# Kernel optimization log

Measured on AMD Instinct MI355X. Metric: run time of the kernel, lower is better.

The kernel has to match this reference:

```python
import jax, jax.numpy as jnp
import numpy as np

EPS_MIN = 1e-8
EPS_MAX = 1.0


def setup_inputs() -> dict:
    key = jax.random.key(0)
    k0, k1, k2, k3 = jax.random.split(key, 4)
    B, H, NT, NV = 8, 16, 512, 576
    return {
        "attn_t_0": jax.random.uniform(k0, (B, H, NT, NV), dtype=jnp.float32),
        "attn_v_0": jax.random.uniform(k1, (B, H, NV, NT), dtype=jnp.float32),
        "attn_t_1": jax.random.uniform(k2, (B, H, NT, NV), dtype=jnp.float32),
        "attn_v_1": jax.random.uniform(k3, (B, H, NV, NT), dtype=jnp.float32),
    }


def _layer_loss(attn_t, attn_v):
    # Head-mean attention maps
    P_t = attn_t.mean(axis=1)  # (B, NT, NV)
    P_v = attn_v.mean(axis=1)  # (B, NV, NT)
    # Only the diagonals of P_t @ P_v and P_v @ P_t are used:
    # diag(A @ B)[b, i] = sum_k A[b, i, k] * B[b, k, i]
    text_diag = jnp.einsum('bik,bki->bi', P_t, P_v)    # (B, NT)
    vision_diag = jnp.einsum('bjk,bkj->bj', P_v, P_t)  # (B, NV)
    text_diag = jnp.clip(text_diag, EPS_MIN, EPS_MAX)
    vision_diag = jnp.clip(vision_diag, EPS_MIN, EPS_MAX)
    loss_text = -jnp.log(text_diag).mean()
    loss_vision = -jnp.log(vision_diag).mean()
    return (loss_text + loss_vision) * 0.5


def reference(attn_t_0, attn_v_0, attn_t_1, attn_v_1) -> jnp.ndarray:
    layers = [(attn_t_0, attn_v_0), (attn_t_1, attn_v_1)]
    total = jnp.float32(0.0)
    for at, av in layers:
        total = total + _layer_loss(at, av)
    return total / len(layers)
```

## Files before the change

### kernel.cpp

```cpp
#include <hip/hip_runtime.h>
#include <math.h>

constexpr int B  = 8;
constexpr int H  = 16;
constexpr int NT = 512;
constexpr int NV = 576;
constexpr int TILE = 64;
constexpr float INV_H2 = 1.0f / (float)(H * H);

constexpr int TEXT_N = 2 * B * NT;
constexpr int VIS_N  = 2 * B * NV;

__global__ void zero_ws_kernel(float* __restrict__ ws, int n) {
    int i = blockIdx.x * blockDim.x + threadIdx.x;
    if (i < n) ws[i] = 0.0f;
}

__global__ __launch_bounds__(256) void fused_diag_kernel(
    const float* __restrict__ t0, const float* __restrict__ v0,
    const float* __restrict__ t1, const float* __restrict__ v1,
    float* __restrict__ text_acc,
    float* __restrict__ vis_acc)
{
    const int ktile = blockIdx.x;
    const int itile = blockIdx.y;
    const int bz    = blockIdx.z;
    const int b     = bz & (B - 1);
    const int layer = bz >> 3;

    const float* __restrict__ T = layer ? t1 : t0;
    const float* __restrict__ V = layer ? v1 : v0;

    const int tid = threadIdx.x;
    const int c = tid & 15;
    const int g = tid >> 4;

    const int i0 = itile * TILE;
    const int k0 = ktile * TILE;

    const size_t tbase = (size_t)b * H * NT * NV + (size_t)i0 * NV + k0;
    const size_t vbase = (size_t)b * H * NV * NT + (size_t)k0 * NT + i0;

    float4 tacc[4];
    float4 vacc[4];
#pragma unroll
    for (int r = 0; r < 4; ++r) {
        tacc[r] = make_float4(0.f, 0.f, 0.f, 0.f);
        vacc[r] = make_float4(0.f, 0.f, 0.f, 0.f);
    }

    for (int h = 0; h < H; ++h) {
        const float* tp = T + tbase + (size_t)h * NT * NV;
        const float* vp = V + vbase + (size_t)h * NV * NT;
#pragma unroll
        for (int r = 0; r < 4; ++r) {
            const int row = g + 16 * r;
            const float4 tv = *(const float4*)(tp + (size_t)row * NV + 4 * c);
            const float4 vv = *(const float4*)(vp + (size_t)row * NT + 4 * c);
            tacc[r].x += tv.x; tacc[r].y += tv.y; tacc[r].z += tv.z; tacc[r].w += tv.w;
            vacc[r].x += vv.x; vacc[r].y += vv.y; vacc[r].z += vv.z; vacc[r].w += vv.w;
        }
    }

    __shared__ float vlds[TILE * 65];
    __shared__ float rowsum[TILE];
    __shared__ float colsum[TILE];

    if (tid < TILE) {
        rowsum[tid] = 0.0f;
        colsum[tid] = 0.0f;
    }

#pragma unroll
    for (int r = 0; r < 4; ++r) {
        const int kk = g + 16 * r;
        float* p = &vlds[kk * 65 + 4 * c];
        p[0] = vacc[r].x; p[1] = vacc[r].y; p[2] = vacc[r].z; p[3] = vacc[r].w;
    }
    __syncthreads();

    float colpart[4] = {0.f, 0.f, 0.f, 0.f};
#pragma unroll
    for (int r = 0; r < 4; ++r) {
        const int ii = g + 16 * r;
        const float tq[4] = {tacc[r].x, tacc[r].y, tacc[r].z, tacc[r].w};
        float rp = 0.f;
#pragma unroll
        for (int j = 0; j < 4; ++j) {
            const int kk = 4 * c + j;
            const float q = tq[j] * vlds[kk * 65 + ii];
            rp += q;
            colpart[j] += q;
        }
        atomicAdd(&rowsum[ii], rp);
    }
#pragma unroll
    for (int j = 0; j < 4; ++j) {
        atomicAdd(&colsum[4 * c + j], colpart[j]);
    }
    __syncthreads();

    const int lb = layer * B + b;
    if (tid < TILE) {
        atomicAdd(&text_acc[(size_t)lb * NT + i0 + tid], rowsum[tid] * INV_H2);
    } else if (tid < 2 * TILE) {
        const int kk = tid - TILE;
        atomicAdd(&vis_acc[(size_t)lb * NV + k0 + kk], colsum[kk] * INV_H2);
    }
}

__global__ __launch_bounds__(256) void finalize_kernel(
    const float* __restrict__ text_acc,
    const float* __restrict__ vis_acc,
    float* __restrict__ out)
{
    const int tid = threadIdx.x;
    const float wt = 0.25f / (float)(B * NT);
    const float wv = 0.25f / (float)(B * NV);

    float s = 0.f;
    for (int i = tid; i < TEXT_N; i += 256) {
        float x = text_acc[i];
        x = fminf(fmaxf(x, 1e-8f), 1.0f);
        s += -logf(x) * wt;
    }
    for (int i = tid; i < VIS_N; i += 256) {
        float x = vis_acc[i];
        x = fminf(fmaxf(x, 1e-8f), 1.0f);
        s += -logf(x) * wv;
    }

#pragma unroll
    for (int off = 32; off > 0; off >>= 1) s += __shfl_down(s, off, 64);

    __shared__ float wsum[4];
    if ((tid & 63) == 0) wsum[tid >> 6] = s;
    __syncthreads();
    if (tid == 0) out[0] = wsum[0] + wsum[1] + wsum[2] + wsum[3];
}

extern "C" void kernel_launch(void* const* d_in, const int* in_sizes, int n_in,
                              void* d_out, int out_size, void* d_ws, size_t ws_size,
                              hipStream_t stream) {
    const float* t0 = (const float*)d_in[0];
    const float* v0 = (const float*)d_in[1];
    const float* t1 = (const float*)d_in[2];
    const float* v1 = (const float*)d_in[3];

    float* text_acc = (float*)d_ws;
    float* vis_acc  = text_acc + TEXT_N;
    float* out      = (float*)d_out;

    {
        const int n = TEXT_N + VIS_N;
        zero_ws_kernel<<<(n + 255) / 256, 256, 0, stream>>>(text_acc, n);
    }

    {
        dim3 grid(NV / TILE, NT / TILE, 2 * B);
        fused_diag_kernel<<<grid, 256, 0, stream>>>(t0, v0, t1, v1, text_acc, vis_acc);
    }

    finalize_kernel<<<1, 256, 0, stream>>>(text_acc, vis_acc, out);
}
```

Baseline: 504.6 us.

## Split head-mean into separate streaming kernel before diagonal product

Head averaging is moved out of the tiled diagonal kernel into a dedicated kernel that streams each input contiguously and writes per-batch head sums to workspace. The diagonal kernel then loads just one precomputed tile per operand instead of looping over heads with strided tile loads. This trades an extra intermediate write/read and an extra launch for more coalesced, bandwidth-friendly reads of the large inputs.

```diff
diff --git a/kernel.cpp b/kernel.cpp
--- a/kernel.cpp
+++ b/kernel.cpp
@@ -6,8 +6,12 @@
 constexpr int NT = 512;
 constexpr int NV = 576;
 constexpr int TILE = 64;
+constexpr int M  = NT * NV;
+constexpr int M4 = M / 4;
+constexpr int OUT4_PER_TENSOR = B * M4;
 constexpr float INV_H2 = 1.0f / (float)(H * H);
 
+constexpr size_t P_FLOATS = (size_t)4 * B * M;
 constexpr int TEXT_N = 2 * B * NT;
 constexpr int VIS_N  = 2 * B * NV;
 
@@ -16,9 +20,34 @@
     if (i < n) ws[i] = 0.0f;
 }
 
-__global__ __launch_bounds__(256) void fused_diag_kernel(
-    const float* __restrict__ t0, const float* __restrict__ v0,
-    const float* __restrict__ t1, const float* __restrict__ v1,
+__global__ __launch_bounds__(256) void mean_kernel(
+    const float4* __restrict__ x0, const float4* __restrict__ x1,
+    const float4* __restrict__ x2, const float4* __restrict__ x3,
+    float4* __restrict__ p)
+{
+    const int o = blockIdx.x * blockDim.x + threadIdx.x;
+    const int t = blockIdx.y;
+    const float4* __restrict__ x = (t == 0) ? x0 : (t == 1) ? x1 : (t == 2) ? x2 : x3;
+
+    const int b  = o / M4;
+    const int m4 = o - b * M4;
+    const float4* __restrict__ src = x + (size_t)b * H * M4 + m4;
+
+    float4 s0 = make_float4(0.f, 0.f, 0.f, 0.f);
+    float4 s1 = make_float4(0.f, 0.f, 0.f, 0.f);
+#pragma unroll
+    for (int h = 0; h < H; h += 2) {
+        const float4 a = src[(size_t)h * M4];
+        const float4 c = src[(size_t)(h + 1) * M4];
+        s0.x += a.x; s0.y += a.y; s0.z += a.z; s0.w += a.w;
+        s1.x += c.x; s1.y += c.y; s1.z += c.z; s1.w += c.w;
+    }
+    s0.x += s1.x; s0.y += s1.y; s0.z += s1.z; s0.w += s1.w;
+    p[(size_t)t * OUT4_PER_TENSOR + o] = s0;
+}
+
+__global__ __launch_bounds__(256) void diag_kernel(
+    const float* __restrict__ P,
     float* __restrict__ text_acc,
     float* __restrict__ vis_acc)
 {
@@ -28,8 +57,8 @@
     const int b     = bz & (B - 1);
     const int layer = bz >> 3;
 
-    const float* __restrict__ T = layer ? t1 : t0;
-    const float* __restrict__ V = layer ? v1 : v0;
+    const float* __restrict__ Pt = P + (size_t)(2 * layer) * B * M + (size_t)b * M;
+    const float* __restrict__ Pv = P + (size_t)(2 * layer + 1) * B * M + (size_t)b * M;
 
     const int tid = threadIdx.x;
     const int c = tid & 15;
@@ -38,28 +67,13 @@
     const int i0 = itile * TILE;
     const int k0 = ktile * TILE;
 
-    const size_t tbase = (size_t)b * H * NT * NV + (size_t)i0 * NV + k0;
-    const size_t vbase = (size_t)b * H * NV * NT + (size_t)k0 * NT + i0;
-
     float4 tacc[4];
     float4 vacc[4];
 #pragma unroll
     for (int r = 0; r < 4; ++r) {
-        tacc[r] = make_float4(0.f, 0.f, 0.f, 0.f);
-        vacc[r] = make_float4(0.f, 0.f, 0.f, 0.f);
-    }
-
-    for (int h = 0; h < H; ++h) {
-        const float* tp = T + tbase + (size_t)h * NT * NV;
-        const float* vp = V + vbase + (size_t)h * NV * NT;
-#pragma unroll
-        for (int r = 0; r < 4; ++r) {
-            const int row = g + 16 * r;
-            const float4 tv = *(const float4*)(tp + (size_t)row * NV + 4 * c);
-            const float4 vv = *(const float4*)(vp + (size_t)row * NT + 4 * c);
-            tacc[r].x += tv.x; tacc[r].y += tv.y; tacc[r].z += tv.z; tacc[r].w += tv.w;
-            vacc[r].x += vv.x; vacc[r].y += vv.y; vacc[r].z += vv.z; vacc[r].w += vv.w;
-        }
+        const int row = g + 16 * r;
+        tacc[r] = *(const float4*)(Pt + (size_t)(i0 + row) * NV + k0 + 4 * c);
+        vacc[r] = *(const float4*)(Pv + (size_t)(k0 + row) * NT + i0 + 4 * c);
     }
 
     __shared__ float vlds[TILE * 65];
@@ -142,12 +156,13 @@
 extern "C" void kernel_launch(void* const* d_in, const int* in_sizes, int n_in,
                               void* d_out, int out_size, void* d_ws, size_t ws_size,
                               hipStream_t stream) {
-    const float* t0 = (const float*)d_in[0];
-    const float* v0 = (const float*)d_in[1];
-    const float* t1 = (const float*)d_in[2];
-    const float* v1 = (const float*)d_in[3];
+    const float4* t0 = (const float4*)d_in[0];
+    const float4* v0 = (const float4*)d_in[1];
+    const float4* t1 = (const float4*)d_in[2];
+    const float4* v1 = (const float4*)d_in[3];
 
-    float* text_acc = (float*)d_ws;
+    float* P        = (float*)d_ws;
+    float* text_acc = P + P_FLOATS;
     float* vis_acc  = text_acc + TEXT_N;
     float* out      = (float*)d_out;
 
@@ -157,8 +172,13 @@
     }
 
     {
+        dim3 grid(OUT4_PER_TENSOR / 256, 4);
+        mean_kernel<<<grid, 256, 0, stream>>>(t0, v0, t1, v1, (float4*)P);
+    }
+
+    {
         dim3 grid(NV / TILE, NT / TILE, 2 * B);
-        fused_diag_kernel<<<grid, 256, 0, stream>>>(t0, v0, t1, v1, text_acc, vis_acc);
+        diag_kernel<<<grid, 256, 0, stream>>>(P, text_acc, vis_acc);
     }
 
     finalize_kernel<<<1, 256, 0, stream>>>(text_acc, vis_acc, out);
```

Result: slower. 515.5 us (+2.1%).
